# Kernel tuning notes

Measured on AMD Instinct MI355X. Metric: run time of the kernel, lower is better.

## Reference

```python
import jax, jax.numpy as jnp
import numpy as np

T, B, H = 2048, 8, 1024


def setup_inputs() -> dict:
    key = jax.random.key(0)
    ks = jax.random.split(key, 4)
    scale = 1.0 / np.sqrt(H)
    x = jax.random.normal(ks[0], (T, B, H), dtype=jnp.float32)
    W_q = jax.random.normal(ks[1], (H, H), dtype=jnp.float32) * scale
    b_q = jnp.zeros((H,), dtype=jnp.float32)
    beta_raw = jax.random.normal(ks[2], (H,), dtype=jnp.float32)
    W_fc = jax.random.normal(ks[3], (H, H), dtype=jnp.float32) * scale
    b_fc = jnp.zeros((H,), dtype=jnp.float32)
    return {"x": x, "W_q": W_q, "b_q": b_q, "beta_raw": beta_raw,
            "W_fc": W_fc, "b_fc": b_fc}


def reference(x, W_q, b_q, beta_raw, W_fc, b_fc):
    # Per-neuron learned leak in (0,1)
    beta = jax.nn.sigmoid(beta_raw)  # (H,)
    # Input (q) projection: (T,B,H) @ (H,H)^T
    q = jnp.einsum('tbh,oh->tbo', x, W_q) + b_q  # (T,B,H)
    # Leaky integration m_t = beta * m_{t-1} + q_t as an associative scan over T
    a = jnp.broadcast_to(beta, q.shape)  # (T,B,H)

    def combine(c1, c2):
        a1, m1 = c1
        a2, m2 = c2
        return (a1 * a2, a2 * m1 + m2)

    _, m = jax.lax.associative_scan(combine, (a, q), axis=0)  # (T,B,H)
    # Linear + ReLU
    h = jnp.einsum('tbh,oh->tbo', m, W_fc) + b_fc
    return jax.nn.relu(h)
```

## Files before the change

kernel.cpp:

```cpp
#include <hip/hip_runtime.h>
#include <stdint.h>

typedef unsigned short u16;
typedef __bf16 bf16x8 __attribute__((ext_vector_type(8)));
typedef float f32x4 __attribute__((ext_vector_type(4)));

__device__ __forceinline__ u16 f2bf(float f) {
  union { float f; uint32_t u; } x; x.f = f;
  uint32_t u = x.u;
  u += 0x7fffu + ((u >> 16) & 1u);
  return (u16)(u >> 16);
}
__device__ __forceinline__ float bf2f(uint32_t lo16) {
  union { uint32_t u; float f; } x; x.u = lo16 << 16; return x.f;
}

__device__ __forceinline__ void async_load16(const u16* g, u16* l) {
  __builtin_amdgcn_global_load_lds(
      (const __attribute__((address_space(1))) void*)g,
      (__attribute__((address_space(3))) void*)l,
      16, 0, 0);
}

__global__ __launch_bounds__(256) void prep(const float* __restrict__ Wq,
                                            const float* __restrict__ Wfc,
                                            const float* __restrict__ braw,
                                            u16* __restrict__ wqb,
                                            u16* __restrict__ wfcb,
                                            float* __restrict__ beta) {
  int gid = blockIdx.x * 256 + threadIdx.x;
  if (gid < 1024) beta[gid] = 1.0f / (1.0f + expf(-braw[gid]));
  const int HH = 1024 * 1024;
  int i = gid * 4;
  if (i < HH) {
    float4 v = *(const float4*)(Wq + i);
    ushort4 o = {f2bf(v.x), f2bf(v.y), f2bf(v.z), f2bf(v.w)};
    *(ushort4*)(wqb + i) = o;
  } else {
    int j = i - HH;
    float4 v = *(const float4*)(Wfc + j);
    ushort4 o = {f2bf(v.x), f2bf(v.y), f2bf(v.z), f2bf(v.w)};
    *(ushort4*)(wfcb + j) = o;
  }
}

__global__ __launch_bounds__(256) void cvt_x8(const float* __restrict__ in,
                                              u16* __restrict__ out, int n) {
  int i = (blockIdx.x * 256 + threadIdx.x) * 8;
  if (i < n) {
    float4 a = *(const float4*)(in + i);
    float4 b = *(const float4*)(in + i + 4);
    ushort4 o0 = {f2bf(a.x), f2bf(a.y), f2bf(a.z), f2bf(a.w)};
    ushort4 o1 = {f2bf(b.x), f2bf(b.y), f2bf(b.z), f2bf(b.w)};
    *(ushort4*)(out + i) = o0;
    *(ushort4*)(out + i + 4) = o1;
  }
}

template <int RELU, int OUTBF>
__global__ __launch_bounds__(256) void gemm_bt(const u16* __restrict__ A,
                                               const u16* __restrict__ B,
                                               const float* __restrict__ bias,
                                               void* __restrict__ Cout,
                                               int M, int N, int K) {
  __shared__ u16 As[128 * 32];
  __shared__ u16 Bs[128 * 32];

  const int tid  = threadIdx.x;
  const int lane = tid & 63;

  const int L  = blockIdx.x;
  const int xc = L & 7;
  const int k8 = L >> 3;
  const int tile_n = (k8 & 7) * 128;
  const int tile_m = ((xc << 4) | (k8 >> 3)) * 128;

  const int wm = ((tid >> 7) & 1) * 64;
  const int wn = ((tid >> 6) & 1) * 64;

  const int srow = tid >> 2;
  const int scol = (((tid & 3) ^ ((tid >> 3) & 3)) << 3);
  u16* ldsA = &As[(tid >> 6) << 9];
  u16* ldsB = &Bs[(tid >> 6) << 9];

  const u16* gA = A + (size_t)(tile_m + srow) * K + scol;
  const u16* gB = B + (size_t)(tile_n + srow) * K + scol;

  f32x4 acc[4][4];
#pragma unroll
  for (int i = 0; i < 4; i++)
#pragma unroll
    for (int j = 0; j < 4; j++) acc[i][j] = (f32x4){0.f, 0.f, 0.f, 0.f};

  const int lrow = lane & 15;
  const int gcq  = lane >> 4;
  const int ccL8 = (gcq ^ ((lrow >> 1) & 3)) << 3;

  for (int k0 = 0; k0 < K; k0 += 32) {
    __syncthreads();
    async_load16(gA + k0, ldsA);
    async_load16(gA + 64 * (size_t)K + k0, ldsA + 2048);
    async_load16(gB + k0, ldsB);
    async_load16(gB + 64 * (size_t)K + k0, ldsB + 2048);
    __syncthreads();

    bf16x8 a[4], b[4];
#pragma unroll
    for (int i = 0; i < 4; i++)
      a[i] = *(const bf16x8*)&As[(wm + i * 16 + lrow) * 32 + ccL8];
#pragma unroll
    for (int j = 0; j < 4; j++)
      b[j] = *(const bf16x8*)&Bs[(wn + j * 16 + lrow) * 32 + ccL8];
#pragma unroll
    for (int i = 0; i < 4; i++)
#pragma unroll
      for (int j = 0; j < 4; j++)
        acc[i][j] = __builtin_amdgcn_mfma_f32_16x16x32_bf16(a[i], b[j], acc[i][j], 0, 0, 0);
  }

  const int crow = (lane >> 4) << 2;
  const int ccol = lane & 15;
#pragma unroll
  for (int i = 0; i < 4; i++) {
#pragma unroll
    for (int j = 0; j < 4; j++) {
      const int gm = tile_m + wm + i * 16 + crow;
      const int gn = tile_n + wn + j * 16 + ccol;
      const float bv = bias[gn];
#pragma unroll
      for (int r = 0; r < 4; r++) {
        float v = acc[i][j][r] + bv;
        if (RELU) v = fmaxf(v, 0.f);
        if (OUTBF) ((u16*)Cout)[(size_t)(gm + r) * N + gn] = f2bf(v);
        else       ((float*)Cout)[(size_t)(gm + r) * N + gn] = v;
      }
    }
  }
}

#define NCH 8192
#define SEG 32
#define NSEG 64

__global__ __launch_bounds__(256) void scan_carry(const uint32_t* __restrict__ qb,
                                                  float* __restrict__ carry,
                                                  const float* __restrict__ beta_arr) {
  int tid = blockIdx.x * 256 + threadIdx.x;
  int seg = tid >> 12;
  int cp  = tid & 4095;
  int h0  = (cp * 2) & 1023;
  float b0 = beta_arr[h0], b1 = beta_arr[h0 + 1];
  const uint32_t* p = qb + (size_t)seg * SEG * 4096 + cp;
  float m0 = 0.f, m1 = 0.f;
#pragma unroll 8
  for (int t = 0; t < SEG; t++) {
    uint32_t v = p[(size_t)t * 4096];
    m0 = fmaf(b0, m0, bf2f(v & 0xffffu));
    m1 = fmaf(b1, m1, bf2f(v >> 16));
  }
  *(float2*)&carry[(size_t)seg * NCH + cp * 2] = make_float2(m0, m1);
}

__global__ __launch_bounds__(256) void carry_scan(float* __restrict__ carry,
                                                  const float* __restrict__ beta_arr) {
  int ch = blockIdx.x * 256 + threadIdx.x;
  float beta = beta_arr[ch & 1023];
  float bseg = beta;
#pragma unroll
  for (int i = 0; i < 5; i++) bseg *= bseg;
  float c[NSEG];
#pragma unroll
  for (int s = 0; s < NSEG; s++) c[s] = carry[(size_t)s * NCH + ch];
  float F = 0.f;
#pragma unroll
  for (int s = 0; s < NSEG; s++) { float t = c[s]; c[s] = F; F = fmaf(bseg, F, t); }
#pragma unroll
  for (int s = 0; s < NSEG; s++) carry[(size_t)s * NCH + ch] = c[s];
}

__global__ __launch_bounds__(256) void scan_out(const uint32_t* __restrict__ qb,
                                                const float* __restrict__ carry,
                                                const float* __restrict__ beta_arr,
                                                uint32_t* __restrict__ mb) {
  int tid = blockIdx.x * 256 + threadIdx.x;
  int seg = tid >> 12;
  int cp  = tid & 4095;
  int h0  = (cp * 2) & 1023;
  float b0 = beta_arr[h0], b1 = beta_arr[h0 + 1];
  float2 F = *(const float2*)&carry[(size_t)seg * NCH + cp * 2];
  float m0 = F.x, m1 = F.y;
  const uint32_t* p = qb + (size_t)seg * SEG * 4096 + cp;
  uint32_t* o = mb + (size_t)seg * SEG * 4096 + cp;
#pragma unroll 8
  for (int t = 0; t < SEG; t++) {
    uint32_t v = p[(size_t)t * 4096];
    m0 = fmaf(b0, m0, bf2f(v & 0xffffu));
    m1 = fmaf(b1, m1, bf2f(v >> 16));
    o[(size_t)t * 4096] = (uint32_t)f2bf(m0) | ((uint32_t)f2bf(m1) << 16);
  }
}

extern "C" void kernel_launch(void* const* d_in, const int* in_sizes, int n_in,
                              void* d_out, int out_size, void* d_ws, size_t ws_size,
                              hipStream_t stream) {
  const float* x        = (const float*)d_in[0];
  const float* W_q      = (const float*)d_in[1];
  const float* b_q      = (const float*)d_in[2];
  const float* beta_raw = (const float*)d_in[3];
  const float* W_fc     = (const float*)d_in[4];
  const float* b_fc     = (const float*)d_in[5];

  const int H = 1024;
  const int M = 2048 * 8;
  const size_t MH = (size_t)M * H;

  char* ws = (char*)d_ws;
  u16* x_bf    = (u16*)ws;  ws += MH * 2;
  u16* q_bf    = (u16*)ws;  ws += MH * 2;
  u16* m_bf    = (u16*)ws;  ws += MH * 2;
  u16* wq_bf   = (u16*)ws;  ws += (size_t)H * H * 2;
  u16* wfc_bf  = (u16*)ws;  ws += (size_t)H * H * 2;
  float* beta  = (float*)ws; ws += 4096;
  float* carry = (float*)ws; ws += (size_t)NSEG * NCH * 4;

  prep<<<2048, 256, 0, stream>>>(W_q, W_fc, beta_raw, wq_bf, wfc_bf, beta);
  cvt_x8<<<(int)(MH / 8 / 256), 256, 0, stream>>>(x, x_bf, (int)MH);

  gemm_bt<0, 1><<<1024, 256, 0, stream>>>(x_bf, wq_bf, b_q, q_bf, M, H, H);

  scan_carry<<<NSEG * (NCH / 2) / 256, 256, 0, stream>>>((const uint32_t*)q_bf, carry, beta);
  carry_scan<<<NCH / 256, 256, 0, stream>>>(carry, beta);
  scan_out<<<NSEG * (NCH / 2) / 256, 256, 0, stream>>>((const uint32_t*)q_bf, carry, beta,
                                                       (uint32_t*)m_bf);

  gemm_bt<1, 0><<<1024, 256, 0, stream>>>(m_bf, wfc_bf, b_fc, d_out, M, H, H);
}
```

Before: 264.3 us.

## Fuse conversion kernels, widen scan accesses, add explicit waitcnt in GEMM

Merges the weight/beta conversion and the x conversion into a single prep_all kernel, which removes one launch. The scan kernels now handle four channels per thread using 8-byte loads and stores, giving fewer threads with wider memory transactions. An explicit s_waitcnt(0) is placed before the barrier in the GEMM k-loop so the async global-to-LDS loads are guaranteed complete. The waitcnt is mostly a correctness guard and may add a small stall; the wider scan cuts the thread count, which lowers parallelism.

```diff
diff --git a/kernel.cpp b/kernel.cpp
--- a/kernel.cpp
+++ b/kernel.cpp
@@ -22,38 +22,36 @@
       16, 0, 0);
 }
 
-__global__ __launch_bounds__(256) void prep(const float* __restrict__ Wq,
-                                            const float* __restrict__ Wfc,
-                                            const float* __restrict__ braw,
-                                            u16* __restrict__ wqb,
-                                            u16* __restrict__ wfcb,
-                                            float* __restrict__ beta) {
+__global__ __launch_bounds__(256) void prep_all(const float* __restrict__ x,
+                                                const float* __restrict__ Wq,
+                                                const float* __restrict__ Wfc,
+                                                const float* __restrict__ braw,
+                                                u16* __restrict__ xb,
+                                                u16* __restrict__ wqb,
+                                                u16* __restrict__ wfcb,
+                                                float* __restrict__ beta) {
   int gid = blockIdx.x * 256 + threadIdx.x;
   if (gid < 1024) beta[gid] = 1.0f / (1.0f + expf(-braw[gid]));
-  const int HH = 1024 * 1024;
-  int i = gid * 4;
-  if (i < HH) {
-    float4 v = *(const float4*)(Wq + i);
-    ushort4 o = {f2bf(v.x), f2bf(v.y), f2bf(v.z), f2bf(v.w)};
-    *(ushort4*)(wqb + i) = o;
-  } else {
-    int j = i - HH;
-    float4 v = *(const float4*)(Wfc + j);
-    ushort4 o = {f2bf(v.x), f2bf(v.y), f2bf(v.z), f2bf(v.w)};
-    *(ushort4*)(wfcb + j) = o;
-  }
-}
-
-__global__ __launch_bounds__(256) void cvt_x8(const float* __restrict__ in,
-                                              u16* __restrict__ out, int n) {
-  int i = (blockIdx.x * 256 + threadIdx.x) * 8;
-  if (i < n) {
-    float4 a = *(const float4*)(in + i);
-    float4 b = *(const float4*)(in + i + 4);
+  if (gid < 131072) {
+    const int HH = 1024 * 1024;
+    int i = gid * 16;
+    const float* src = (i < HH) ? (Wq + i) : (Wfc + (i - HH));
+    u16* dst = (i < HH) ? (wqb + i) : (wfcb + (i - HH));
+#pragma unroll
+    for (int c = 0; c < 4; c++) {
+      float4 v = *(const float4*)(src + c * 4);
+      ushort4 o = {f2bf(v.x), f2bf(v.y), f2bf(v.z), f2bf(v.w)};
+      *(ushort4*)(dst + c * 4) = o;
+    }
+  }
+  {
+    int i = gid * 8;
+    float4 a = *(const float4*)(x + i);
+    float4 b = *(const float4*)(x + i + 4);
     ushort4 o0 = {f2bf(a.x), f2bf(a.y), f2bf(a.z), f2bf(a.w)};
     ushort4 o1 = {f2bf(b.x), f2bf(b.y), f2bf(b.z), f2bf(b.w)};
-    *(ushort4*)(out + i) = o0;
-    *(ushort4*)(out + i + 4) = o1;
+    *(ushort4*)(xb + i) = o0;
+    *(ushort4*)(xb + i + 4) = o1;
   }
 }
 
@@ -102,6 +100,7 @@
     async_load16(gA + 64 * (size_t)K + k0, ldsA + 2048);
     async_load16(gB + k0, ldsB);
     async_load16(gB + 64 * (size_t)K + k0, ldsB + 2048);
+    __builtin_amdgcn_s_waitcnt(0);
     __syncthreads();
 
     bf16x8 a[4], b[4];
@@ -142,23 +141,25 @@
 #define SEG 32
 #define NSEG 64
 
-__global__ __launch_bounds__(256) void scan_carry(const uint32_t* __restrict__ qb,
+__global__ __launch_bounds__(256) void scan_carry(const uint2* __restrict__ qb,
                                                   float* __restrict__ carry,
                                                   const float* __restrict__ beta_arr) {
   int tid = blockIdx.x * 256 + threadIdx.x;
-  int seg = tid >> 12;
-  int cp  = tid & 4095;
-  int h0  = (cp * 2) & 1023;
-  float b0 = beta_arr[h0], b1 = beta_arr[h0 + 1];
-  const uint32_t* p = qb + (size_t)seg * SEG * 4096 + cp;
-  float m0 = 0.f, m1 = 0.f;
+  int seg = tid >> 11;
+  int cq  = tid & 2047;
+  int h0  = (cq * 4) & 1023;
+  float b0 = beta_arr[h0], b1 = beta_arr[h0 + 1], b2 = beta_arr[h0 + 2], b3 = beta_arr[h0 + 3];
+  const uint2* p = qb + (size_t)seg * SEG * 2048 + cq;
+  float m0 = 0.f, m1 = 0.f, m2 = 0.f, m3 = 0.f;
 #pragma unroll 8
   for (int t = 0; t < SEG; t++) {
-    uint32_t v = p[(size_t)t * 4096];
-    m0 = fmaf(b0, m0, bf2f(v & 0xffffu));
-    m1 = fmaf(b1, m1, bf2f(v >> 16));
-  }
-  *(float2*)&carry[(size_t)seg * NCH + cp * 2] = make_float2(m0, m1);
+    uint2 v = p[(size_t)t * 2048];
+    m0 = fmaf(b0, m0, bf2f(v.x & 0xffffu));
+    m1 = fmaf(b1, m1, bf2f(v.x >> 16));
+    m2 = fmaf(b2, m2, bf2f(v.y & 0xffffu));
+    m3 = fmaf(b3, m3, bf2f(v.y >> 16));
+  }
+  *(float4*)&carry[(size_t)seg * NCH + cq * 4] = make_float4(m0, m1, m2, m3);
 }
 
 __global__ __launch_bounds__(256) void carry_scan(float* __restrict__ carry,
@@ -178,25 +179,30 @@
   for (int s = 0; s < NSEG; s++) carry[(size_t)s * NCH + ch] = c[s];
 }
 
-__global__ __launch_bounds__(256) void scan_out(const uint32_t* __restrict__ qb,
+__global__ __launch_bounds__(256) void scan_out(const uint2* __restrict__ qb,
                                                 const float* __restrict__ carry,
                                                 const float* __restrict__ beta_arr,
-                                                uint32_t* __restrict__ mb) {
+                                                uint2* __restrict__ mb) {
   int tid = blockIdx.x * 256 + threadIdx.x;
-  int seg = tid >> 12;
-  int cp  = tid & 4095;
-  int h0  = (cp * 2) & 1023;
-  float b0 = beta_arr[h0], b1 = beta_arr[h0 + 1];
-  float2 F = *(const float2*)&carry[(size_t)seg * NCH + cp * 2];
-  float m0 = F.x, m1 = F.y;
-  const uint32_t* p = qb + (size_t)seg * SEG * 4096 + cp;
-  uint32_t* o = mb + (size_t)seg * SEG * 4096 + cp;
+  int seg = tid >> 11;
+  int cq  = tid & 2047;
+  int h0  = (cq * 4) & 1023;
+  float b0 = beta_arr[h0], b1 = beta_arr[h0 + 1], b2 = beta_arr[h0 + 2], b3 = beta_arr[h0 + 3];
+  float4 F = *(const float4*)&carry[(size_t)seg * NCH + cq * 4];
+  float m0 = F.x, m1 = F.y, m2 = F.z, m3 = F.w;
+  const uint2* p = qb + (size_t)seg * SEG * 2048 + cq;
+  uint2* o = mb + (size_t)seg * SEG * 2048 + cq;
 #pragma unroll 8
   for (int t = 0; t < SEG; t++) {
-    uint32_t v = p[(size_t)t * 4096];
-    m0 = fmaf(b0, m0, bf2f(v & 0xffffu));
-    m1 = fmaf(b1, m1, bf2f(v >> 16));
-    o[(size_t)t * 4096] = (uint32_t)f2bf(m0) | ((uint32_t)f2bf(m1) << 16);
+    uint2 v = p[(size_t)t * 2048];
+    m0 = fmaf(b0, m0, bf2f(v.x & 0xffffu));
+    m1 = fmaf(b1, m1, bf2f(v.x >> 16));
+    m2 = fmaf(b2, m2, bf2f(v.y & 0xffffu));
+    m3 = fmaf(b3, m3, bf2f(v.y >> 16));
+    uint2 w;
+    w.x = (uint32_t)f2bf(m0) | ((uint32_t)f2bf(m1) << 16);
+    w.y = (uint32_t)f2bf(m2) | ((uint32_t)f2bf(m3) << 16);
+    o[(size_t)t * 2048] = w;
   }
 }
 
@@ -223,15 +229,15 @@
   float* beta  = (float*)ws; ws += 4096;
   float* carry = (float*)ws; ws += (size_t)NSEG * NCH * 4;
 
-  prep<<<2048, 256, 0, stream>>>(W_q, W_fc, beta_raw, wq_bf, wfc_bf, beta);
-  cvt_x8<<<(int)(MH / 8 / 256), 256, 0, stream>>>(x, x_bf, (int)MH);
+  prep_all<<<(int)(MH / 8 / 256), 256, 0, stream>>>(x, W_q, W_fc, beta_raw,
+                                                    x_bf, wq_bf, wfc_bf, beta);
 
   gemm_bt<0, 1><<<1024, 256, 0, stream>>>(x_bf, wq_bf, b_q, q_bf, M, H, H);
 
-  scan_carry<<<NSEG * (NCH / 2) / 256, 256, 0, stream>>>((const uint32_t*)q_bf, carry, beta);
+  scan_carry<<<NSEG * (NCH / 4) / 256, 256, 0, stream>>>((const uint2*)q_bf, carry, beta);
   carry_scan<<<NCH / 256, 256, 0, stream>>>(carry, beta);
-  scan_out<<<NSEG * (NCH / 2) / 256, 256, 0, stream>>>((const uint32_t*)q_bf, carry, beta,
-                                                       (uint32_t*)m_bf);
+  scan_out<<<NSEG * (NCH / 4) / 256, 256, 0, stream>>>((const uint2*)q_bf, carry, beta,
+                                                       (uint2*)m_bf);
 
   gemm_bt<1, 0><<<1024, 256, 0, stream>>>(m_bf, wfc_bf, b_fc, d_out, M, H, H);
 }
```

After: 263.7 us. No clear change (-0.2%).
